# Kernel optimization log

Hardware: AMD Instinct MI355X
Metric: run time of the kernel (lower is better)

## Reference

```python
import jax, jax.numpy as jnp
import numpy as np

BASE_T = 0.07
ALPHA = 0.5
EPS = 1e-12  # torch F.normalize eps


def _l2_normalize(x):
    norm = jnp.linalg.norm(x, axis=1, keepdims=True)
    return x / jnp.maximum(norm, EPS)


def setup_inputs() -> dict:
    key = jax.random.key(0)
    k1, k2, k3 = jax.random.split(key, 3)
    B, D, H, W = 4096, 512, 16, 16
    return {
        "emb1": jax.random.normal(k1, (B, D), dtype=jnp.float32),
        "emb2": jax.random.normal(k2, (B, D), dtype=jnp.float32),
        "attention_map": jax.random.uniform(k3, (B, H, W), dtype=jnp.float32),
    }


def reference(emb1, emb2, attention_map):
    B = emb1.shape[0]
    e1 = _l2_normalize(emb1)
    e2 = _l2_normalize(emb2)

    att = attention_map.mean(axis=(1, 2))                     # [B]
    temp = (BASE_T * (1.0 + ALPHA * att))[:, None]            # [B, 1]

    x = jnp.concatenate([e1, e2], axis=0)                     # [2B, D]
    x_swap = jnp.concatenate([e2, e1], axis=0)                # [2B, D]
    temp_cat = jnp.concatenate([temp, temp], axis=0)          # [2B, 1]

    sim = jnp.matmul(x, x.T) / temp_cat                       # [2B, 2B]
    pos_sim = jnp.sum(x * x_swap, axis=1) / temp_cat[:, 0]    # [2B]

    diag = jnp.eye(2 * B, dtype=bool)
    sim = jnp.where(diag, -jnp.inf, sim)                      # exp(-inf) = 0

    denominator = jnp.exp(sim).sum(axis=1)                    # [2B]
    loss = -jnp.log(jnp.exp(pos_sim) / denominator)
    return loss.mean()
```

## Files before the change

### kernel.cpp

```cpp
#include <hip/hip_runtime.h>
#include <hip/hip_bf16.h>
#include <math.h>

#define B_ROWS 4096
#define D_DIM 512
#define TWO_B 8192
#define HW_N 256
#define BASE_T 0.07f
#define ALPHA_C 0.5f
#define LOG2E 1.44269504088896340736f

typedef float v4f __attribute__((ext_vector_type(4)));

__device__ __forceinline__ float fast_exp2(float x) {
#if __has_builtin(__builtin_amdgcn_exp2f)
    return __builtin_amdgcn_exp2f(x);
#else
    return exp2f(x);
#endif
}

__global__ __launch_bounds__(256) void prep_kernel(
    const float* __restrict__ emb1, const float* __restrict__ emb2,
    const float* __restrict__ att, unsigned short* __restrict__ X8,
    float* __restrict__ inv_temp, float* __restrict__ pos)
{
    const int b = blockIdx.x;
    const int t = threadIdx.x;
    const float2 a1 = ((const float2*)(emb1 + (size_t)b * D_DIM))[t];
    const float2 a2 = ((const float2*)(emb2 + (size_t)b * D_DIM))[t];
    float av = att[(size_t)b * HW_N + t];
    float s1  = a1.x * a1.x + a1.y * a1.y;
    float s2  = a2.x * a2.x + a2.y * a2.y;
    float s12 = a1.x * a2.x + a1.y * a2.y;
    #pragma unroll
    for (int m = 1; m < 64; m <<= 1) {
        s1  += __shfl_xor(s1, m, 64);
        s2  += __shfl_xor(s2, m, 64);
        s12 += __shfl_xor(s12, m, 64);
        av  += __shfl_xor(av, m, 64);
    }
    __shared__ float red[4][4];
    const int w = t >> 6, lane = t & 63;
    if (lane == 0) { red[w][0] = s1; red[w][1] = s2; red[w][2] = s12; red[w][3] = av; }
    __syncthreads();
    const float T1  = red[0][0] + red[1][0] + red[2][0] + red[3][0];
    const float T2  = red[0][1] + red[1][1] + red[2][1] + red[3][1];
    const float T12 = red[0][2] + red[1][2] + red[2][2] + red[3][2];
    const float Ta  = red[0][3] + red[1][3] + red[2][3] + red[3][3];
    const float i1 = 1.0f / fmaxf(sqrtf(T1), 1e-12f);
    const float i2 = 1.0f / fmaxf(sqrtf(T2), 1e-12f);
    const float it = 1.0f / (BASE_T * (1.0f + ALPHA_C * (Ta * (1.0f / 256.0f))));
    const int p1 = __builtin_amdgcn_cvt_pk_fp8_f32(a1.x * i1, a1.y * i1, 0, false);
    const int p2 = __builtin_amdgcn_cvt_pk_fp8_f32(a2.x * i2, a2.y * i2, 0, false);
    X8[(size_t)b * 256 + t]            = (unsigned short)(p1 & 0xffff);
    X8[(size_t)(b + B_ROWS) * 256 + t] = (unsigned short)(p2 & 0xffff);
    if (t == 0) {
        inv_temp[b] = it * LOG2E;
        inv_temp[b + B_ROWS] = it * LOG2E;
        pos[b] = (T12 * i1 * i2) * it;
    }
}

__device__ __forceinline__ void gload_lds16(const void* g, void* s) {
    __builtin_amdgcn_global_load_lds(
        (const __attribute__((address_space(1))) unsigned int*)g,
        (__attribute__((address_space(3))) unsigned int*)s,
        16, 0, 0);
}

__global__ __launch_bounds__(256) void gram_kernel(
    const unsigned char* __restrict__ X8,
    const float* __restrict__ inv_temp,
    float* __restrict__ partial)
{
    const int bid = (blockIdx.x & 7) * 260 + (blockIdx.x >> 3);
    int rb = (int)((129.0f - sqrtf(129.0f * 129.0f - 8.0f * (float)bid)) * 0.5f);
    rb = rb < 0 ? 0 : (rb > 63 ? 63 : rb);
    while (rb > 0 && (rb * (129 - rb)) / 2 > bid) rb--;
    while (rb < 63 && ((rb + 1) * (129 - (rb + 1))) / 2 <= bid) rb++;
    const int cb = rb + (bid - (rb * (129 - rb)) / 2);

    __shared__ unsigned char smA[128 * 256];
    __shared__ unsigned char smB[128 * 256];

    const int rowBase = rb * 128;
    const int colBase = cb * 128;

    const int tid  = threadIdx.x;
    const int w    = tid >> 6;
    const int lane = tid & 63;
    const int quad = lane >> 4;
    const int t    = lane & 15;
    const int wm   = w >> 1;
    const int wn   = w & 1;

    const int srow   = lane >> 4;
    const int schunk = lane & 15;

    const unsigned char* Arow0 = X8 + (size_t)rowBase * D_DIM;
    const unsigned char* Brow0 = X8 + (size_t)colBase * D_DIM;

    v4f acc[4][4];
    #pragma unroll
    for (int a = 0; a < 4; a++)
        #pragma unroll
        for (int b2 = 0; b2 < 4; b2++)
            acc[a][b2] = v4f{0.0f, 0.0f, 0.0f, 0.0f};

    for (int p = 0; p < 2; p++) {
        const int kk = p * 256;
        #pragma unroll
        for (int j = 0; j < 8; j++) {
            const int g = w * 8 + j;
            const int r = g * 4 + srow;
            const int gc = schunk ^ (r & 15);
            gload_lds16(Arow0 + (size_t)r * D_DIM + kk + gc * 16, &smA[g * 1024]);
            gload_lds16(Brow0 + (size_t)r * D_DIM + kk + gc * 16, &smB[g * 1024]);
        }
        __syncthreads();

        #pragma unroll
        for (int s = 0; s < 8; s++) {
            const int pu = (s * 2 + (quad >> 1)) ^ t;
            const int off = pu * 16 + (quad & 1) * 8;
            long aF[4], bF[4];
            #pragma unroll
            for (int mi = 0; mi < 4; mi++)
                aF[mi] = *(const long*)&smA[(wm * 64 + mi * 16 + t) * 256 + off];
            #pragma unroll
            for (int ni = 0; ni < 4; ni++)
                bF[ni] = *(const long*)&smB[(wn * 64 + ni * 16 + t) * 256 + off];
            #pragma unroll
            for (int mi = 0; mi < 4; mi++)
                #pragma unroll
                for (int ni = 0; ni < 4; ni++)
                    acc[mi][ni] = __builtin_amdgcn_mfma_f32_16x16x32_fp8_fp8(
                        aF[mi], bF[ni], acc[mi][ni], 0, 0, 0);
        }
        if (p == 0) __syncthreads();
    }

    v4f itv[4];
    #pragma unroll
    for (int mi = 0; mi < 4; mi++)
        itv[mi] = *(const v4f*)&inv_temp[rowBase + wm * 64 + mi * 16 + quad * 4];

    float* prow = partial + (size_t)(cb * 2 + wn) * TWO_B;
    #pragma unroll
    for (int mi = 0; mi < 4; mi++) {
        #pragma unroll
        for (int r = 0; r < 4; r++) {
            const int i = rowBase + wm * 64 + mi * 16 + quad * 4 + r;
            const float it = itv[mi][r];
            float s = 0.0f;
            #pragma unroll
            for (int ni = 0; ni < 4; ni++) {
                const int j = colBase + wn * 64 + ni * 16 + t;
                const float v = fast_exp2(acc[mi][ni][r] * it);
                s += (i == j) ? 0.0f : v;
            }
            s += __shfl_xor(s, 1, 64);
            s += __shfl_xor(s, 2, 64);
            s += __shfl_xor(s, 4, 64);
            s += __shfl_xor(s, 8, 64);
            if (t == 0) prow[i] = s;
        }
    }

    if (rb != cb) {
        float itj[4];
        float cs[4] = {0.0f, 0.0f, 0.0f, 0.0f};
        #pragma unroll
        for (int ni = 0; ni < 4; ni++)
            itj[ni] = inv_temp[colBase + wn * 64 + ni * 16 + t];
        #pragma unroll
        for (int mi = 0; mi < 4; mi++)
            #pragma unroll
            for (int r = 0; r < 4; r++)
                #pragma unroll
                for (int ni = 0; ni < 4; ni++)
                    cs[ni] += fast_exp2(acc[mi][ni][r] * itj[ni]);
        float* pcol = partial + (size_t)(rb * 2 + wm) * TWO_B;
        #pragma unroll
        for (int ni = 0; ni < 4; ni++) {
            cs[ni] += __shfl_xor(cs[ni], 16, 64);
            cs[ni] += __shfl_xor(cs[ni], 32, 64);
            if (quad == 0) pcol[colBase + wn * 64 + ni * 16 + t] = cs[ni];
        }
    }
}

__global__ __launch_bounds__(256) void finish1(
    const float* __restrict__ partial, const float* __restrict__ pos,
    float* __restrict__ blockSums)
{
    const int i = blockIdx.x * 256 + threadIdx.x;
    float d = 0.0f;
    #pragma unroll 8
    for (int s = 0; s < 128; s++) d += partial[(size_t)s * TWO_B + i];
    float li = logf(d) - pos[i & (B_ROWS - 1)];
    #pragma unroll
    for (int m = 1; m < 64; m <<= 1) li += __shfl_xor(li, m, 64);
    __shared__ float red[4];
    const int w = threadIdx.x >> 6, lane = threadIdx.x & 63;
    if (lane == 0) red[w] = li;
    __syncthreads();
    if (threadIdx.x == 0) blockSums[blockIdx.x] = red[0] + red[1] + red[2] + red[3];
}

__global__ void finish2(const float* __restrict__ blockSums, float* __restrict__ out)
{
    const int lane = threadIdx.x;
    float v = (lane < 32) ? blockSums[lane] : 0.0f;
    #pragma unroll
    for (int m = 1; m < 64; m <<= 1) v += __shfl_xor(v, m, 64);
    if (lane == 0) out[0] = v * (1.0f / 8192.0f);
}

extern "C" void kernel_launch(void* const* d_in, const int* in_sizes, int n_in,
                              void* d_out, int out_size, void* d_ws, size_t ws_size,
                              hipStream_t stream) {
    const float* emb1 = (const float*)d_in[0];
    const float* emb2 = (const float*)d_in[1];
    const float* att  = (const float*)d_in[2];
    float* out = (float*)d_out;

    char* ws = (char*)d_ws;
    unsigned short* X8 = (unsigned short*)ws;
    float* inv_temp    = (float*)(ws + 4194304);
    float* pos         = (float*)(ws + 4194304 + 32768);
    float* partial     = (float*)(ws + 4194304 + 32768 + 16384);
    float* blockSums   = (float*)(ws + 4194304 + 32768 + 16384 + 4194304);

    prep_kernel<<<B_ROWS, 256, 0, stream>>>(emb1, emb2, att, X8, inv_temp, pos);
    gram_kernel<<<2080, 256, 0, stream>>>((const unsigned char*)X8, inv_temp, partial);
    finish1<<<TWO_B / 256, 256, 0, stream>>>(partial, pos, blockSums);
    finish2<<<1, 64, 0, stream>>>(blockSums, out);
}
```

Before: 129.0 us.

## Enlarge Gram tiles to 256x256 with double-buffered K pipeline

The Gram kernel switches from 128x128 upper-triangle tiles with 256 threads to 256x256 tiles with 512 threads, using 128 KB of dynamic LDS. That LDS holds two A/B buffers staged over four K chunks, so the next chunk loads while the current one computes. The goal is to reuse each loaded fp8 tile across more MFMAs and hide global-to-LDS latency. Row and column partial sums now go to separate buffers, and the finish kernel reads only the populated entries. The cost is one block per CU and fewer, larger blocks (528), which can leave a load-imbalance tail and fewer resident waves for hiding the exp epilogue.

```diff
diff --git a/kernel.cpp b/kernel.cpp
--- a/kernel.cpp
+++ b/kernel.cpp
@@ -69,23 +69,24 @@
         16, 0, 0);
 }
 
-__global__ __launch_bounds__(256) void gram_kernel(
+__global__ __launch_bounds__(512, 2) void gram_kernel(
     const unsigned char* __restrict__ X8,
     const float* __restrict__ inv_temp,
-    float* __restrict__ partial)
-{
-    const int bid = (blockIdx.x & 7) * 260 + (blockIdx.x >> 3);
-    int rb = (int)((129.0f - sqrtf(129.0f * 129.0f - 8.0f * (float)bid)) * 0.5f);
-    rb = rb < 0 ? 0 : (rb > 63 ? 63 : rb);
-    while (rb > 0 && (rb * (129 - rb)) / 2 > bid) rb--;
-    while (rb < 63 && ((rb + 1) * (129 - (rb + 1))) / 2 <= bid) rb++;
-    const int cb = rb + (bid - (rb * (129 - rb)) / 2);
-
-    __shared__ unsigned char smA[128 * 256];
-    __shared__ unsigned char smB[128 * 256];
-
-    const int rowBase = rb * 128;
-    const int colBase = cb * 128;
+    float* __restrict__ partialR,
+    float* __restrict__ partialC)
+{
+    extern __shared__ unsigned char sm[];
+
+    const int raw = blockIdx.x;
+    const int bid = (raw & 7) * 66 + (raw >> 3);
+    int h = (int)((65.0f - sqrtf(65.0f * 65.0f - 8.0f * (float)bid)) * 0.5f);
+    h = h < 0 ? 0 : (h > 31 ? 31 : h);
+    while (h > 0 && (h * (65 - h)) / 2 > bid) h--;
+    while (h < 31 && ((h + 1) * (64 - h)) / 2 <= bid) h++;
+    const int g = h + (bid - (h * (65 - h)) / 2);
+
+    const int rowBase = h * 256;
+    const int colBase = g * 256;
 
     const int tid  = threadIdx.x;
     const int w    = tid >> 6;
@@ -95,58 +96,89 @@
     const int wm   = w >> 1;
     const int wn   = w & 1;
 
-    const int srow   = lane >> 4;
-    const int schunk = lane & 15;
+    const int srow = lane >> 3;
+    const int sc   = lane & 7;
+    const int gcx  = sc ^ srow;
 
     const unsigned char* Arow0 = X8 + (size_t)rowBase * D_DIM;
     const unsigned char* Brow0 = X8 + (size_t)colBase * D_DIM;
 
-    v4f acc[4][4];
+    unsigned char* const bA0 = sm;
+    unsigned char* const bB0 = sm + 32768;
+    unsigned char* const bA1 = sm + 65536;
+    unsigned char* const bB1 = sm + 98304;
+
+    v4f acc[4][8];
     #pragma unroll
     for (int a = 0; a < 4; a++)
         #pragma unroll
-        for (int b2 = 0; b2 < 4; b2++)
+        for (int b2 = 0; b2 < 8; b2++)
             acc[a][b2] = v4f{0.0f, 0.0f, 0.0f, 0.0f};
 
-    for (int p = 0; p < 2; p++) {
-        const int kk = p * 256;
-        #pragma unroll
-        for (int j = 0; j < 8; j++) {
-            const int g = w * 8 + j;
-            const int r = g * 4 + srow;
-            const int gc = schunk ^ (r & 15);
-            gload_lds16(Arow0 + (size_t)r * D_DIM + kk + gc * 16, &smA[g * 1024]);
-            gload_lds16(Brow0 + (size_t)r * D_DIM + kk + gc * 16, &smB[g * 1024]);
-        }
-        __syncthreads();
-
-        #pragma unroll
-        for (int s = 0; s < 8; s++) {
-            const int pu = (s * 2 + (quad >> 1)) ^ t;
-            const int off = pu * 16 + (quad & 1) * 8;
-            long aF[4], bF[4];
-            #pragma unroll
-            for (int mi = 0; mi < 4; mi++)
-                aF[mi] = *(const long*)&smA[(wm * 64 + mi * 16 + t) * 256 + off];
-            #pragma unroll
-            for (int ni = 0; ni < 4; ni++)
-                bF[ni] = *(const long*)&smB[(wn * 64 + ni * 16 + t) * 256 + off];
-            #pragma unroll
-            for (int mi = 0; mi < 4; mi++)
-                #pragma unroll
-                for (int ni = 0; ni < 4; ni++)
-                    acc[mi][ni] = __builtin_amdgcn_mfma_f32_16x16x32_fp8_fp8(
-                        aF[mi], bF[ni], acc[mi][ni], 0, 0, 0);
-        }
-        if (p == 0) __syncthreads();
-    }
+#define STAGE(PH, BA, BB)                                                     \
+    {                                                                         \
+        const int kk = (PH) * 128;                                            \
+        _Pragma("unroll")                                                     \
+        for (int j = 0; j < 4; j++) {                                         \
+            const int ga = w * 4 + j;                \
+            const int r = ga * 8 + srow;                          \
+            gload_lds16(Arow0 + (size_t)r * D_DIM + kk + gcx * 16,            \
+                        (BA) + ga * 1024);                                    \
+            gload_lds16(Brow0 + (size_t)r * D_DIM + kk + gcx * 16,            \
+                        (BB) + ga * 1024);                                    \
+        }                                                                     \
+    }
+
+#define COMPUTE(BA, BB)                                                       \
+    {                                                                         \
+        _Pragma("unroll")                                                     \
+        for (int s = 0; s < 4; s++) {                                         \
+            const int u = s * 2 + (quad >> 1);                                \
+            const int half = (quad & 1) * 8;                                  \
+            long aF[4], bF[8];                                                \
+            _Pragma("unroll")                                                 \
+            for (int mi = 0; mi < 4; mi++) {                                  \
+                const int row = wm * 64 + mi * 16 + t;                        \
+                const int pu = u ^ (row & 7);                                 \
+                aF[mi] = *(const long*)&(BA)[row * 128 + pu * 16 + half];     \
+            }                                                                 \
+            _Pragma("unroll")                                                 \
+            for (int ni = 0; ni < 8; ni++) {                                  \
+                const int col = wn * 128 + ni * 16 + t;                       \
+                const int pu = u ^ (col & 7);                                 \
+                bF[ni] = *(const long*)&(BB)[col * 128 + pu * 16 + half];     \
+            }                                                                 \
+            _Pragma("unroll")                                                 \
+            for (int mi = 0; mi < 4; mi++)                                    \
+                _Pragma("unroll")                                             \
+                for (int ni = 0; ni < 8; ni++)                                \
+                    acc[mi][ni] = __builtin_amdgcn_mfma_f32_16x16x32_fp8_fp8( \
+                        aF[mi], bF[ni], acc[mi][ni], 0, 0, 0);                \
+        }                                                                     \
+    }
+
+    STAGE(0, bA0, bB0)
+    __syncthreads();
+    STAGE(1, bA1, bB1)
+    COMPUTE(bA0, bB0)
+    __syncthreads();
+    STAGE(2, bA0, bB0)
+    COMPUTE(bA1, bB1)
+    __syncthreads();
+    STAGE(3, bA1, bB1)
+    COMPUTE(bA0, bB0)
+    __syncthreads();
+    COMPUTE(bA1, bB1)
+
+#undef STAGE
+#undef COMPUTE
 
     v4f itv[4];
     #pragma unroll
     for (int mi = 0; mi < 4; mi++)
         itv[mi] = *(const v4f*)&inv_temp[rowBase + wm * 64 + mi * 16 + quad * 4];
 
-    float* prow = partial + (size_t)(cb * 2 + wn) * TWO_B;
+    float* pR = partialR + (size_t)(g * 2 + wn) * TWO_B;
     #pragma unroll
     for (int mi = 0; mi < 4; mi++) {
         #pragma unroll
@@ -155,8 +187,8 @@
             const float it = itv[mi][r];
             float s = 0.0f;
             #pragma unroll
-            for (int ni = 0; ni < 4; ni++) {
-                const int j = colBase + wn * 64 + ni * 16 + t;
+            for (int ni = 0; ni < 8; ni++) {
+                const int j = colBase + wn * 128 + ni * 16 + t;
                 const float v = fast_exp2(acc[mi][ni][r] * it);
                 s += (i == j) ? 0.0f : v;
             }
@@ -164,41 +196,39 @@
             s += __shfl_xor(s, 2, 64);
             s += __shfl_xor(s, 4, 64);
             s += __shfl_xor(s, 8, 64);
-            if (t == 0) prow[i] = s;
+            if (t == 0) pR[i] = s;
         }
     }
 
-    if (rb != cb) {
-        float itj[4];
-        float cs[4] = {0.0f, 0.0f, 0.0f, 0.0f};
+    if (h != g) {
+        float* pC = partialC + (size_t)(h * 4 + wm) * TWO_B;
         #pragma unroll
-        for (int ni = 0; ni < 4; ni++)
-            itj[ni] = inv_temp[colBase + wn * 64 + ni * 16 + t];
-        #pragma unroll
-        for (int mi = 0; mi < 4; mi++)
+        for (int ni = 0; ni < 8; ni++) {
+            const int j = colBase + wn * 128 + ni * 16 + t;
+            const float itj = inv_temp[j];
+            float cs = 0.0f;
             #pragma unroll
-            for (int r = 0; r < 4; r++)
+            for (int mi = 0; mi < 4; mi++)
                 #pragma unroll
-                for (int ni = 0; ni < 4; ni++)
-                    cs[ni] += fast_exp2(acc[mi][ni][r] * itj[ni]);
-        float* pcol = partial + (size_t)(rb * 2 + wm) * TWO_B;
-        #pragma unroll
-        for (int ni = 0; ni < 4; ni++) {
-            cs[ni] += __shfl_xor(cs[ni], 16, 64);
-            cs[ni] += __shfl_xor(cs[ni], 32, 64);
-            if (quad == 0) pcol[colBase + wn * 64 + ni * 16 + t] = cs[ni];
+                for (int r = 0; r < 4; r++)
+                    cs += fast_exp2(acc[mi][ni][r] * itj);
+            cs += __shfl_xor(cs, 16, 64);
+            cs += __shfl_xor(cs, 32, 64);
+            if (quad == 0) pC[j] = cs;
         }
     }
 }
 
 __global__ __launch_bounds__(256) void finish1(
-    const float* __restrict__ partial, const float* __restrict__ pos,
-    float* __restrict__ blockSums)
+    const float* __restrict__ partialR, const float* __restrict__ partialC,
+    const float* __restrict__ pos, float* __restrict__ blockSums)
 {
     const int i = blockIdx.x * 256 + threadIdx.x;
+    const int gi = i >> 8;
     float d = 0.0f;
-    #pragma unroll 8
-    for (int s = 0; s < 128; s++) d += partial[(size_t)s * TWO_B + i];
+    for (int c = 2 * gi; c < 64; c++) d += partialR[(size_t)c * TWO_B + i];
+    const int smax = 4 * gi;
+    for (int s = 0; s < smax; s++) d += partialC[(size_t)s * TWO_B + i];
     float li = logf(d) - pos[i & (B_ROWS - 1)];
     #pragma unroll
     for (int m = 1; m < 64; m <<= 1) li += __shfl_xor(li, m, 64);
@@ -229,12 +259,21 @@
     char* ws = (char*)d_ws;
     unsigned short* X8 = (unsigned short*)ws;
     float* inv_temp    = (float*)(ws + 4194304);
-    float* pos         = (float*)(ws + 4194304 + 32768);
-    float* partial     = (float*)(ws + 4194304 + 32768 + 16384);
-    float* blockSums   = (float*)(ws + 4194304 + 32768 + 16384 + 4194304);
+    float* pos         = (float*)(ws + 4227072);
+    float* partialR    = (float*)(ws + 4243456);
+    float* partialC    = (float*)(ws + 6340608);
+    float* blockSums   = (float*)(ws + 10534912);
+
+    static bool attr_set = false;
+    if (!attr_set) {
+        hipFuncSetAttribute((const void*)gram_kernel,
+                            hipFuncAttributeMaxDynamicSharedMemorySize, 131072);
+        attr_set = true;
+    }
 
     prep_kernel<<<B_ROWS, 256, 0, stream>>>(emb1, emb2, att, X8, inv_temp, pos);
-    gram_kernel<<<2080, 256, 0, stream>>>((const unsigned char*)X8, inv_temp, partial);
-    finish1<<<TWO_B / 256, 256, 0, stream>>>(partial, pos, blockSums);
+    gram_kernel<<<528, 512, 131072, stream>>>((const unsigned char*)X8,
+                                              inv_temp, partialR, partialC);
+    finish1<<<TWO_B / 256, 256, 0, stream>>>(partialR, partialC, pos, blockSums);
     finish2<<<1, 64, 0, stream>>>(blockSums, out);
 }
```

New measurement: 156.3 us. 21.2% more time.
